# Optimization experiments

Hardware: AMD Instinct MI355X
Metric: run time of the kernel (lower is better)

Reference implementation:

```python
import jax, jax.numpy as jnp
import numpy as np

BN_EPS = 1e-5


def setup_inputs() -> dict:
    key = jax.random.key(0)
    ks = jax.random.split(key, 8)
    N, Cin, Cout, D, H, W = 4, 512, 256, 256, 128, 128
    feat_ffm = jax.random.normal(ks[0], (N, Cin, H, W), dtype=jnp.float32)
    coarse_x = jax.random.normal(ks[1], (N, D, H, W), dtype=jnp.float32)
    # conv1: 1x1, no bias; BN (eval mode: running stats); conv2: 1x1 with bias
    w1 = jax.random.normal(ks[2], (Cout, Cin), dtype=jnp.float32) * (1.0 / np.sqrt(Cin))
    bn_gamma = jnp.ones((Cout,), dtype=jnp.float32)
    bn_beta = jnp.zeros((Cout,), dtype=jnp.float32)
    bn_mean = jax.random.normal(ks[3], (Cout,), dtype=jnp.float32) * 0.1
    bn_var = jax.random.uniform(ks[4], (Cout,), dtype=jnp.float32, minval=0.5, maxval=1.5)
    w2 = jax.random.normal(ks[5], (Cout, Cout), dtype=jnp.float32) * (1.0 / np.sqrt(Cout))
    b2 = jnp.zeros((Cout,), dtype=jnp.float32)
    return {"feat_ffm": feat_ffm, "coarse_x": coarse_x, "w1": w1,
            "bn_gamma": bn_gamma, "bn_beta": bn_beta, "bn_mean": bn_mean,
            "bn_var": bn_var, "w2": w2, "b2": b2}


def reference(feat_ffm, coarse_x, w1, bn_gamma, bn_beta, bn_mean, bn_var, w2, b2):
    N, D, H, W = coarse_x.shape
    # conv1 (1x1) + BN(eval) + ReLU; Dropout2d is identity in eval mode
    x = jnp.einsum('nihw,oi->nohw', feat_ffm, w1)
    scale = bn_gamma * jax.lax.rsqrt(bn_var + BN_EPS)
    x = x * scale[None, :, None, None] + (bn_beta - bn_mean * scale)[None, :, None, None]
    x = jax.nn.relu(x)  # [N, C, H, W]
    C = x.shape[1]
    q = coarse_x.reshape(N, D, H * W)          # proj_query / proj_value
    k = x.reshape(N, C, H * W)                 # proj_key (pre-permute)
    energy = jnp.einsum('nds,ncs->ndc', q, k)  # [N, D, C]
    energy_new = jnp.max(energy, axis=-1, keepdims=True) - energy
    attention = jax.nn.softmax(energy_new, axis=-1)        # [N, D, C]
    out = jnp.einsum('ndc,nds->ncs', attention, q)         # attention^T @ value
    out = out.reshape(N, C, H, W)
    out = jnp.einsum('nchw,oc->nohw', out, w2) + b2[None, :, None, None]
    return out
```

## Files before the change

### kernel.cpp

```cpp
#include <hip/hip_runtime.h>


#define S_DIM 16384
#define C_DIM 256
#define CIN 512

typedef unsigned short u16;
typedef __attribute__((ext_vector_type(8))) short bf16x8;
typedef __attribute__((ext_vector_type(4))) float f32x4;

__device__ __forceinline__ u16 f2bf(float x) {
    unsigned u = __float_as_uint(x);
    u += 0x7fff + ((u >> 16) & 1);
    return (u16)(u >> 16);
}
__device__ __forceinline__ float bf2f(u16 h) {
    return __uint_as_float(((unsigned)h) << 16);
}
__device__ __forceinline__ void gld16(const u16* g, u16* l) {
    __builtin_amdgcn_global_load_lds((const __attribute__((address_space(1))) void*)g,
                                     (__attribute__((address_space(3))) void*)l, 16, 0, 0);
}
__device__ __forceinline__ void gld4(const float* g, float* l) {
    __builtin_amdgcn_global_load_lds((const __attribute__((address_space(1))) void*)g,
                                     (__attribute__((address_space(3))) void*)l, 4, 0, 0);
}

__global__ __launch_bounds__(256) void prep_kernel(
    const float* __restrict__ coarse, const float* __restrict__ w1,
    const float* __restrict__ gamma, const float* __restrict__ beta,
    const float* __restrict__ mean, const float* __restrict__ var,
    u16* __restrict__ qhi, u16* __restrict__ qlo,
    u16* __restrict__ w1hi, u16* __restrict__ w1lo, float* __restrict__ b1) {
    int b = blockIdx.x;
    int t = threadIdx.x;
    if (b < 4096) {
        size_t i = (size_t)b * 256 + t;
        for (size_t c = i; c < 4194304u; c += 1048576u) {
            float4 v = ((const float4*)coarse)[c];
            float vv[4] = {v.x, v.y, v.z, v.w};
            u16 h[4], l[4];
#pragma unroll
            for (int j = 0; j < 4; ++j) {
                h[j] = f2bf(vv[j]);
                l[j] = f2bf(vv[j] - bf2f(h[j]));
            }
            *(uint2*)&qhi[c * 4] = *(uint2*)h;
            *(uint2*)&qlo[c * 4] = *(uint2*)l;
        }
    } else {
        int o = (b - 4096) * 16 + (t >> 4);
        int lane16 = t & 15;
        float sc = gamma[o] * rsqrtf(var[o] + 1e-5f);
        for (int i = lane16; i < CIN; i += 16) {
            float v = w1[o * CIN + i] * sc;
            u16 h = f2bf(v);
            w1hi[o * CIN + i] = h;
            w1lo[o * CIN + i] = f2bf(v - bf2f(h));
        }
        if (lane16 == 0) b1[o] = beta[o] - mean[o] * sc;
    }
}

__global__ __launch_bounds__(256) void conv_kernel(
    const u16* __restrict__ w1hi, const u16* __restrict__ w1lo,
    const float* __restrict__ feat, const float* __restrict__ b1,
    u16* __restrict__ khi, u16* __restrict__ klo) {
    __shared__ u16 AhS[4096], AlS[4096];
    __shared__ float BfS[32 * 133];
    int s0 = blockIdx.x * 128;
    int m0 = blockIdx.y * 128;
    int bz = blockIdx.z;
    int tid = threadIdx.x, wave = tid >> 6, lane = tid & 63;

    int c0 = wave * 128 + lane, c1 = c0 + 64;
    int r0 = c0 >> 2, k0 = (c0 & 3) * 8;
    int r1 = c1 >> 2, k1 = (c1 & 3) * 8;
    const u16* gA0h = w1hi + (size_t)(m0 + r0) * CIN + k0;
    const u16* gA1h = w1hi + (size_t)(m0 + r1) * CIN + k1;
    const u16* gA0l = w1lo + (size_t)(m0 + r0) * CIN + k0;
    const u16* gA1l = w1lo + (size_t)(m0 + r1) * CIN + k1;
    const float* fB = feat + (size_t)bz * ((size_t)CIN * S_DIM) + s0 + lane;

    int quad = lane >> 4, l15 = lane & 15;
    int wm = wave >> 1, wn = wave & 1;
    int aBase = (wm * 64 + l15) * 32 + quad * 8;

    f32x4 zero = {0.f, 0.f, 0.f, 0.f};
    f32x4 acc[4][4];
#pragma unroll
    for (int i = 0; i < 4; ++i)
#pragma unroll
        for (int j = 0; j < 4; ++j) acc[i][j] = zero;

    for (int kb = 0; kb < CIN; kb += 32) {
        __syncthreads();
        gld16(gA0h, AhS + c0 * 8);
        gld16(gA1h, AhS + c1 * 8);
        gld16(gA0l, AlS + c0 * 8);
        gld16(gA1l, AlS + c1 * 8);
        gA0h += 32; gA1h += 32; gA0l += 32; gA1l += 32;
#pragma unroll
        for (int j = 0; j < 16; ++j) {
            int cc = wave * 16 + j;
            int i = cc >> 1, h = cc & 1;
            gld4(fB + (size_t)(kb + i) * S_DIM + h * 64, BfS + i * 133 + h * 64 + lane);
        }
        __syncthreads();

        bf16x8 a_h[4], a_l[4];
#pragma unroll
        for (int t = 0; t < 4; ++t) {
            a_h[t] = *(const bf16x8*)&AhS[aBase + t * 512];
            a_l[t] = *(const bf16x8*)&AlS[aBase + t * 512];
        }
        bf16x8 b_h[4], b_l[4];
#pragma unroll
        for (int nt = 0; nt < 4; ++nt) {
            int n = wn * 64 + nt * 16 + l15;
            union { u16 u[8]; bf16x8 v; } th, tl;
#pragma unroll
            for (int j = 0; j < 8; ++j) {
                float f = BfS[(quad * 8 + j) * 133 + n];
                u16 h = f2bf(f);
                th.u[j] = h;
                tl.u[j] = (u16)(__float_as_uint(f - bf2f(h)) >> 16);
            }
            b_h[nt] = th.v;
            b_l[nt] = tl.v;
        }
#pragma unroll
        for (int mt = 0; mt < 4; ++mt)
#pragma unroll
            for (int nt = 0; nt < 4; ++nt) {
                acc[mt][nt] = __builtin_amdgcn_mfma_f32_16x16x32_bf16(a_h[mt], b_h[nt], acc[mt][nt], 0, 0, 0);
                acc[mt][nt] = __builtin_amdgcn_mfma_f32_16x16x32_bf16(a_h[mt], b_l[nt], acc[mt][nt], 0, 0, 0);
                acc[mt][nt] = __builtin_amdgcn_mfma_f32_16x16x32_bf16(a_l[mt], b_h[nt], acc[mt][nt], 0, 0, 0);
            }
    }

#pragma unroll
    for (int mt = 0; mt < 4; ++mt) {
#pragma unroll
        for (int r = 0; r < 4; ++r) {
            int row = m0 + wm * 64 + mt * 16 + quad * 4 + r;
            float bi = b1[row];
#pragma unroll
            for (int nt = 0; nt < 4; ++nt) {
                int cc = s0 + wn * 64 + nt * 16 + l15;
                float v = fmaxf(acc[mt][nt][r] + bi, 0.f);
                u16 h = f2bf(v);
                size_t o = (size_t)bz * 4194304 + (size_t)row * S_DIM + cc;
                khi[o] = h;
                klo[o] = f2bf(v - bf2f(h));
            }
        }
    }
}

__global__ __launch_bounds__(256) void energy_kernel(
    const u16* __restrict__ qhi, const u16* __restrict__ qlo,
    const u16* __restrict__ khi, const u16* __restrict__ klo,
    float* __restrict__ Ep) {
    __shared__ u16 AhS[4096], BhS[4096], AlS[4096], BlS[4096];
    int kBeg = blockIdx.x * 256;
    int m0 = (blockIdx.y >> 1) * 128;
    int n0 = (blockIdx.y & 1) * 128;
    int bz = blockIdx.z;
    int tid = threadIdx.x, wave = tid >> 6, lane = tid & 63;

    int c0 = wave * 128 + lane, c1 = c0 + 64;
    int r0 = c0 >> 2, k0 = (c0 & 3) * 8;
    int r1 = c1 >> 2, k1 = (c1 & 3) * 8;
    size_t bo = (size_t)bz * 4194304;
    const u16* gA0h = qhi + bo + (size_t)(m0 + r0) * S_DIM + kBeg + k0;
    const u16* gA1h = qhi + bo + (size_t)(m0 + r1) * S_DIM + kBeg + k1;
    const u16* gB0h = khi + bo + (size_t)(n0 + r0) * S_DIM + kBeg + k0;
    const u16* gB1h = khi + bo + (size_t)(n0 + r1) * S_DIM + kBeg + k1;
    const u16* gA0l = qlo + bo + (size_t)(m0 + r0) * S_DIM + kBeg + k0;
    const u16* gA1l = qlo + bo + (size_t)(m0 + r1) * S_DIM + kBeg + k1;
    const u16* gB0l = klo + bo + (size_t)(n0 + r0) * S_DIM + kBeg + k0;
    const u16* gB1l = klo + bo + (size_t)(n0 + r1) * S_DIM + kBeg + k1;

    int quad = lane >> 4, l15 = lane & 15;
    int wm = wave >> 1, wn = wave & 1;
    int aBase = (wm * 64 + l15) * 32 + quad * 8;
    int bBase = (wn * 64 + l15) * 32 + quad * 8;

    f32x4 zero = {0.f, 0.f, 0.f, 0.f};
    f32x4 acc[4][4];
#pragma unroll
    for (int i = 0; i < 4; ++i)
#pragma unroll
        for (int j = 0; j < 4; ++j) acc[i][j] = zero;

    for (int kb = 0; kb < 256; kb += 32) {
        __syncthreads();
        gld16(gA0h, AhS + c0 * 8);
        gld16(gA1h, AhS + c1 * 8);
        gld16(gB0h, BhS + c0 * 8);
        gld16(gB1h, BhS + c1 * 8);
        gld16(gA0l, AlS + c0 * 8);
        gld16(gA1l, AlS + c1 * 8);
        gld16(gB0l, BlS + c0 * 8);
        gld16(gB1l, BlS + c1 * 8);
        gA0h += 32; gA1h += 32; gB0h += 32; gB1h += 32;
        gA0l += 32; gA1l += 32; gB0l += 32; gB1l += 32;
        __syncthreads();

        bf16x8 a_h[4], b_h[4], a_l[4], b_l[4];
#pragma unroll
        for (int t = 0; t < 4; ++t) {
            a_h[t] = *(const bf16x8*)&AhS[aBase + t * 512];
            b_h[t] = *(const bf16x8*)&BhS[bBase + t * 512];
            a_l[t] = *(const bf16x8*)&AlS[aBase + t * 512];
            b_l[t] = *(const bf16x8*)&BlS[bBase + t * 512];
        }
#pragma unroll
        for (int mt = 0; mt < 4; ++mt)
#pragma unroll
            for (int nt = 0; nt < 4; ++nt) {
                acc[mt][nt] = __builtin_amdgcn_mfma_f32_16x16x32_bf16(a_h[mt], b_h[nt], acc[mt][nt], 0, 0, 0);
                acc[mt][nt] = __builtin_amdgcn_mfma_f32_16x16x32_bf16(a_h[mt], b_l[nt], acc[mt][nt], 0, 0, 0);
                acc[mt][nt] = __builtin_amdgcn_mfma_f32_16x16x32_bf16(a_l[mt], b_h[nt], acc[mt][nt], 0, 0, 0);
            }
    }

    float* Ce = Ep + ((size_t)(blockIdx.x * 4 + bz)) * 65536;
#pragma unroll
    for (int mt = 0; mt < 4; ++mt)
#pragma unroll
        for (int r = 0; r < 4; ++r) {
            int row = m0 + wm * 64 + mt * 16 + quad * 4 + r;
#pragma unroll
            for (int nt = 0; nt < 4; ++nt) {
                int cc = n0 + wn * 64 + nt * 16 + l15;
                Ce[(size_t)row * C_DIM + cc] = acc[mt][nt][r];
            }
        }
}

__global__ __launch_bounds__(256) void softmax_kernel(const float* __restrict__ Ep,
                                                      float* __restrict__ att) {
    __shared__ float red[4], red2[4];
    int b = blockIdx.x;
    int t = threadIdx.x;
    const float* p = Ep + (size_t)b * 256 + t;
    float v = 0.f;
#pragma unroll 8
    for (int s = 0; s < 64; ++s) v += p[(size_t)s * 262144];
    float m = v;
#pragma unroll
    for (int o = 32; o > 0; o >>= 1) m = fminf(m, __shfl_xor(m, o, 64));
    int lane = t & 63, wid = t >> 6;
    if (lane == 0) red[wid] = m;
    __syncthreads();
    m = fminf(fminf(red[0], red[1]), fminf(red[2], red[3]));
    float e = expf(m - v);
    float s = e;
#pragma unroll
    for (int o = 32; o > 0; o >>= 1) s += __shfl_xor(s, o, 64);
    if (lane == 0) red2[wid] = s;
    __syncthreads();
    s = red2[0] + red2[1] + red2[2] + red2[3];
    att[(size_t)b * 256 + t] = e / s;
}

__global__ __launch_bounds__(256) void m2h_kernel(const float* __restrict__ w2,
                                                  const float* __restrict__ att,
                                                  u16* __restrict__ M2h) {
    int t = blockIdx.x * 256 + threadIdx.x;
    int d = t & 255, o = (t >> 8) & 255, n = t >> 16;
    const float4* wr = (const float4*)(w2 + (size_t)o * C_DIM);
    const float4* ar = (const float4*)(att + ((size_t)n * C_DIM + d) * C_DIM);
    float s = 0.0f;
#pragma unroll 4
    for (int c4 = 0; c4 < 64; ++c4) {
        float4 w = wr[c4];
        float4 a = ar[c4];
        s += w.x * a.x + w.y * a.y + w.z * a.z + w.w * a.w;
    }
    M2h[((size_t)n * C_DIM + o) * C_DIM + d] = f2bf(s);
}

__global__ __launch_bounds__(256) void final_kernel(
    const u16* __restrict__ M2h, const float* __restrict__ coarse,
    const float* __restrict__ b2, float* __restrict__ out) {
    __shared__ u16 AhS[4096];
    __shared__ float BfS[32 * 133];
    int s0 = blockIdx.x * 128;
    int m0 = blockIdx.y * 128;
    int bz = blockIdx.z;
    int tid = threadIdx.x, wave = tid >> 6, lane = tid & 63;

    int c0 = wave * 128 + lane, c1 = c0 + 64;
    int r0 = c0 >> 2, k0 = (c0 & 3) * 8;
    int r1 = c1 >> 2, k1 = (c1 & 3) * 8;
    const u16* gA0 = M2h + (size_t)bz * 65536 + (size_t)(m0 + r0) * C_DIM + k0;
    const u16* gA1 = M2h + (size_t)bz * 65536 + (size_t)(m0 + r1) * C_DIM + k1;
    const float* fB = coarse + (size_t)bz * 4194304 + s0 + lane;

    int quad = lane >> 4, l15 = lane & 15;
    int wm = wave >> 1, wn = wave & 1;
    int aBase = (wm * 64 + l15) * 32 + quad * 8;

    f32x4 zero = {0.f, 0.f, 0.f, 0.f};
    f32x4 acc[4][4];
#pragma unroll
    for (int i = 0; i < 4; ++i)
#pragma unroll
        for (int j = 0; j < 4; ++j) acc[i][j] = zero;

    for (int kb = 0; kb < C_DIM; kb += 32) {
        __syncthreads();
        gld16(gA0, AhS + c0 * 8);
        gld16(gA1, AhS + c1 * 8);
        gA0 += 32; gA1 += 32;
#pragma unroll
        for (int j = 0; j < 16; ++j) {
            int cc = wave * 16 + j;
            int i = cc >> 1, h = cc & 1;
            gld4(fB + (size_t)(kb + i) * S_DIM + h * 64, BfS + i * 133 + h * 64 + lane);
        }
        __syncthreads();

        bf16x8 a_h[4];
#pragma unroll
        for (int t = 0; t < 4; ++t) a_h[t] = *(const bf16x8*)&AhS[aBase + t * 512];
        bf16x8 b_h[4];
#pragma unroll
        for (int nt = 0; nt < 4; ++nt) {
            int n = wn * 64 + nt * 16 + l15;
            union { u16 u[8]; bf16x8 v; } th;
#pragma unroll
            for (int j = 0; j < 8; ++j) th.u[j] = f2bf(BfS[(quad * 8 + j) * 133 + n]);
            b_h[nt] = th.v;
        }
#pragma unroll
        for (int mt = 0; mt < 4; ++mt)
#pragma unroll
            for (int nt = 0; nt < 4; ++nt)
                acc[mt][nt] = __builtin_amdgcn_mfma_f32_16x16x32_bf16(a_h[mt], b_h[nt], acc[mt][nt], 0, 0, 0);
    }

#pragma unroll
    for (int mt = 0; mt < 4; ++mt)
#pragma unroll
        for (int r = 0; r < 4; ++r) {
            int row = m0 + wm * 64 + mt * 16 + quad * 4 + r;
            float bi = b2[row];
#pragma unroll
            for (int nt = 0; nt < 4; ++nt) {
                int cc = s0 + wn * 64 + nt * 16 + l15;
                out[(size_t)bz * 4194304 + (size_t)row * S_DIM + cc] = acc[mt][nt][r] + bi;
            }
        }
}

extern "C" void kernel_launch(void* const* d_in, const int* in_sizes, int n_in,
                              void* d_out, int out_size, void* d_ws, size_t ws_size,
                              hipStream_t stream) {
    const float* feat   = (const float*)d_in[0];
    const float* coarse = (const float*)d_in[1];
    const float* w1     = (const float*)d_in[2];
    const float* gamma  = (const float*)d_in[3];
    const float* beta   = (const float*)d_in[4];
    const float* mean   = (const float*)d_in[5];
    const float* var    = (const float*)d_in[6];
    const float* w2     = (const float*)d_in[7];
    const float* b2     = (const float*)d_in[8];
    float* out = (float*)d_out;

    char* base = (char*)d_ws;
    u16* qhi   = (u16*)(base);
    u16* qlo   = (u16*)(base + 33554432);
    u16* khi   = (u16*)(base + 67108864);
    u16* klo   = (u16*)(base + 100663296);
    float* Ep  = (float*)(base + 134217728);
    float* att = (float*)(base + 201326592);
    u16* M2h   = (u16*)(base + 202375168);
    u16* w1hi  = (u16*)(base + 202899456);
    u16* w1lo  = (u16*)(base + 203161600);
    float* b1  = (float*)(base + 203423744);

    prep_kernel<<<4112, 256, 0, stream>>>(coarse, w1, gamma, beta, mean, var,
                                          qhi, qlo, w1hi, w1lo, b1);

    conv_kernel<<<dim3(128, 2, 4), 256, 0, stream>>>(w1hi, w1lo, feat, b1, khi, klo);

    energy_kernel<<<dim3(64, 4, 4), 256, 0, stream>>>(qhi, qlo, khi, klo, Ep);

    softmax_kernel<<<1024, 256, 0, stream>>>(Ep, att);

    m2h_kernel<<<1024, 256, 0, stream>>>(w2, att, M2h);

    final_kernel<<<dim3(128, 2, 4), 256, 0, stream>>>(M2h, coarse, b2, out);
}
```

Baseline: 447.5 us.

## Replace LDS staging with direct global loads into MFMA registers

The three GEMM kernels (conv, energy, final) no longer stage operand tiles through shared memory with global_load_lds and barriers. Each lane now loads its MFMA fragments straight from global memory, and the conv kernel's hi/lo split of the fp32 input uses truncation instead of round-to-nearest for the hi part. This removes the LDS traffic and the barriers, but each wave re-reads data from global memory that other waves in the block also load, so more pressure falls on L2. The column-strided fp32 loads issue as many scalar loads per lane.

```diff
diff --git a/kernel.cpp b/kernel.cpp
--- a/kernel.cpp
+++ b/kernel.cpp
@@ -16,14 +16,6 @@
 }
 __device__ __forceinline__ float bf2f(u16 h) {
     return __uint_as_float(((unsigned)h) << 16);
-}
-__device__ __forceinline__ void gld16(const u16* g, u16* l) {
-    __builtin_amdgcn_global_load_lds((const __attribute__((address_space(1))) void*)g,
-                                     (__attribute__((address_space(3))) void*)l, 16, 0, 0);
-}
-__device__ __forceinline__ void gld4(const float* g, float* l) {
-    __builtin_amdgcn_global_load_lds((const __attribute__((address_space(1))) void*)g,
-                                     (__attribute__((address_space(3))) void*)l, 4, 0, 0);
 }
 
 __global__ __launch_bounds__(256) void prep_kernel(
@@ -66,25 +58,17 @@
     const u16* __restrict__ w1hi, const u16* __restrict__ w1lo,
     const float* __restrict__ feat, const float* __restrict__ b1,
     u16* __restrict__ khi, u16* __restrict__ klo) {
-    __shared__ u16 AhS[4096], AlS[4096];
-    __shared__ float BfS[32 * 133];
     int s0 = blockIdx.x * 128;
     int m0 = blockIdx.y * 128;
     int bz = blockIdx.z;
     int tid = threadIdx.x, wave = tid >> 6, lane = tid & 63;
-
-    int c0 = wave * 128 + lane, c1 = c0 + 64;
-    int r0 = c0 >> 2, k0 = (c0 & 3) * 8;
-    int r1 = c1 >> 2, k1 = (c1 & 3) * 8;
-    const u16* gA0h = w1hi + (size_t)(m0 + r0) * CIN + k0;
-    const u16* gA1h = w1hi + (size_t)(m0 + r1) * CIN + k1;
-    const u16* gA0l = w1lo + (size_t)(m0 + r0) * CIN + k0;
-    const u16* gA1l = w1lo + (size_t)(m0 + r1) * CIN + k1;
-    const float* fB = feat + (size_t)bz * ((size_t)CIN * S_DIM) + s0 + lane;
-
     int quad = lane >> 4, l15 = lane & 15;
     int wm = wave >> 1, wn = wave & 1;
-    int aBase = (wm * 64 + l15) * 32 + quad * 8;
+
+    const u16* aH = w1hi + (size_t)(m0 + wm * 64 + l15) * CIN + quad * 8;
+    const u16* aL = w1lo + (size_t)(m0 + wm * 64 + l15) * CIN + quad * 8;
+    const float* fB = feat + (size_t)bz * ((size_t)CIN * S_DIM) +
+                      (size_t)(quad * 8) * S_DIM + s0 + wn * 64 + l15;
 
     f32x4 zero = {0.f, 0.f, 0.f, 0.f};
     f32x4 acc[4][4];
@@ -94,35 +78,22 @@
         for (int j = 0; j < 4; ++j) acc[i][j] = zero;
 
     for (int kb = 0; kb < CIN; kb += 32) {
-        __syncthreads();
-        gld16(gA0h, AhS + c0 * 8);
-        gld16(gA1h, AhS + c1 * 8);
-        gld16(gA0l, AlS + c0 * 8);
-        gld16(gA1l, AlS + c1 * 8);
-        gA0h += 32; gA1h += 32; gA0l += 32; gA1l += 32;
-#pragma unroll
-        for (int j = 0; j < 16; ++j) {
-            int cc = wave * 16 + j;
-            int i = cc >> 1, h = cc & 1;
-            gld4(fB + (size_t)(kb + i) * S_DIM + h * 64, BfS + i * 133 + h * 64 + lane);
-        }
-        __syncthreads();
-
         bf16x8 a_h[4], a_l[4];
 #pragma unroll
-        for (int t = 0; t < 4; ++t) {
-            a_h[t] = *(const bf16x8*)&AhS[aBase + t * 512];
-            a_l[t] = *(const bf16x8*)&AlS[aBase + t * 512];
-        }
+        for (int mt = 0; mt < 4; ++mt) {
+            a_h[mt] = *(const bf16x8*)&aH[(size_t)(mt * 16) * CIN + kb];
+            a_l[mt] = *(const bf16x8*)&aL[(size_t)(mt * 16) * CIN + kb];
+        }
+        const float* fk = fB + (size_t)kb * S_DIM;
         bf16x8 b_h[4], b_l[4];
 #pragma unroll
         for (int nt = 0; nt < 4; ++nt) {
-            int n = wn * 64 + nt * 16 + l15;
             union { u16 u[8]; bf16x8 v; } th, tl;
 #pragma unroll
             for (int j = 0; j < 8; ++j) {
-                float f = BfS[(quad * 8 + j) * 133 + n];
-                u16 h = f2bf(f);
+                float f = fk[(size_t)j * S_DIM + nt * 16];
+                unsigned u = __float_as_uint(f);
+                u16 h = (u16)(u >> 16);
                 th.u[j] = h;
                 tl.u[j] = (u16)(__float_as_uint(f - bf2f(h)) >> 16);
             }
@@ -140,7 +111,7 @@
     }
 
 #pragma unroll
-    for (int mt = 0; mt < 4; ++mt) {
+    for (int mt = 0; mt < 4; ++mt)
 #pragma unroll
         for (int r = 0; r < 4; ++r) {
             int row = m0 + wm * 64 + mt * 16 + quad * 4 + r;
@@ -155,37 +126,25 @@
                 klo[o] = f2bf(v - bf2f(h));
             }
         }
-    }
 }
 
 __global__ __launch_bounds__(256) void energy_kernel(
     const u16* __restrict__ qhi, const u16* __restrict__ qlo,
     const u16* __restrict__ khi, const u16* __restrict__ klo,
     float* __restrict__ Ep) {
-    __shared__ u16 AhS[4096], BhS[4096], AlS[4096], BlS[4096];
     int kBeg = blockIdx.x * 256;
     int m0 = (blockIdx.y >> 1) * 128;
     int n0 = (blockIdx.y & 1) * 128;
     int bz = blockIdx.z;
     int tid = threadIdx.x, wave = tid >> 6, lane = tid & 63;
-
-    int c0 = wave * 128 + lane, c1 = c0 + 64;
-    int r0 = c0 >> 2, k0 = (c0 & 3) * 8;
-    int r1 = c1 >> 2, k1 = (c1 & 3) * 8;
-    size_t bo = (size_t)bz * 4194304;
-    const u16* gA0h = qhi + bo + (size_t)(m0 + r0) * S_DIM + kBeg + k0;
-    const u16* gA1h = qhi + bo + (size_t)(m0 + r1) * S_DIM + kBeg + k1;
-    const u16* gB0h = khi + bo + (size_t)(n0 + r0) * S_DIM + kBeg + k0;
-    const u16* gB1h = khi + bo + (size_t)(n0 + r1) * S_DIM + kBeg + k1;
-    const u16* gA0l = qlo + bo + (size_t)(m0 + r0) * S_DIM + kBeg + k0;
-    const u16* gA1l = qlo + bo + (size_t)(m0 + r1) * S_DIM + kBeg + k1;
-    const u16* gB0l = klo + bo + (size_t)(n0 + r0) * S_DIM + kBeg + k0;
-    const u16* gB1l = klo + bo + (size_t)(n0 + r1) * S_DIM + kBeg + k1;
-
     int quad = lane >> 4, l15 = lane & 15;
     int wm = wave >> 1, wn = wave & 1;
-    int aBase = (wm * 64 + l15) * 32 + quad * 8;
-    int bBase = (wn * 64 + l15) * 32 + quad * 8;
+
+    size_t bo = (size_t)bz * 4194304;
+    const u16* aH = qhi + bo + (size_t)(m0 + wm * 64 + l15) * S_DIM + kBeg + quad * 8;
+    const u16* aL = qlo + bo + (size_t)(m0 + wm * 64 + l15) * S_DIM + kBeg + quad * 8;
+    const u16* bH = khi + bo + (size_t)(n0 + wn * 64 + l15) * S_DIM + kBeg + quad * 8;
+    const u16* bL = klo + bo + (size_t)(n0 + wn * 64 + l15) * S_DIM + kBeg + quad * 8;
 
     f32x4 zero = {0.f, 0.f, 0.f, 0.f};
     f32x4 acc[4][4];
@@ -195,26 +154,13 @@
         for (int j = 0; j < 4; ++j) acc[i][j] = zero;
 
     for (int kb = 0; kb < 256; kb += 32) {
-        __syncthreads();
-        gld16(gA0h, AhS + c0 * 8);
-        gld16(gA1h, AhS + c1 * 8);
-        gld16(gB0h, BhS + c0 * 8);
-        gld16(gB1h, BhS + c1 * 8);
-        gld16(gA0l, AlS + c0 * 8);
-        gld16(gA1l, AlS + c1 * 8);
-        gld16(gB0l, BlS + c0 * 8);
-        gld16(gB1l, BlS + c1 * 8);
-        gA0h += 32; gA1h += 32; gB0h += 32; gB1h += 32;
-        gA0l += 32; gA1l += 32; gB0l += 32; gB1l += 32;
-        __syncthreads();
-
-        bf16x8 a_h[4], b_h[4], a_l[4], b_l[4];
+        bf16x8 a_h[4], a_l[4], b_h[4], b_l[4];
 #pragma unroll
         for (int t = 0; t < 4; ++t) {
-            a_h[t] = *(const bf16x8*)&AhS[aBase + t * 512];
-            b_h[t] = *(const bf16x8*)&BhS[bBase + t * 512];
-            a_l[t] = *(const bf16x8*)&AlS[aBase + t * 512];
-            b_l[t] = *(const bf16x8*)&BlS[bBase + t * 512];
+            a_h[t] = *(const bf16x8*)&aH[(size_t)(t * 16) * S_DIM + kb];
+            a_l[t] = *(const bf16x8*)&aL[(size_t)(t * 16) * S_DIM + kb];
+            b_h[t] = *(const bf16x8*)&bH[(size_t)(t * 16) * S_DIM + kb];
+            b_l[t] = *(const bf16x8*)&bL[(size_t)(t * 16) * S_DIM + kb];
         }
 #pragma unroll
         for (int mt = 0; mt < 4; ++mt)
@@ -286,23 +232,16 @@
 __global__ __launch_bounds__(256) void final_kernel(
     const u16* __restrict__ M2h, const float* __restrict__ coarse,
     const float* __restrict__ b2, float* __restrict__ out) {
-    __shared__ u16 AhS[4096];
-    __shared__ float BfS[32 * 133];
     int s0 = blockIdx.x * 128;
     int m0 = blockIdx.y * 128;
     int bz = blockIdx.z;
     int tid = threadIdx.x, wave = tid >> 6, lane = tid & 63;
-
-    int c0 = wave * 128 + lane, c1 = c0 + 64;
-    int r0 = c0 >> 2, k0 = (c0 & 3) * 8;
-    int r1 = c1 >> 2, k1 = (c1 & 3) * 8;
-    const u16* gA0 = M2h + (size_t)bz * 65536 + (size_t)(m0 + r0) * C_DIM + k0;
-    const u16* gA1 = M2h + (size_t)bz * 65536 + (size_t)(m0 + r1) * C_DIM + k1;
-    const float* fB = coarse + (size_t)bz * 4194304 + s0 + lane;
-
     int quad = lane >> 4, l15 = lane & 15;
     int wm = wave >> 1, wn = wave & 1;
-    int aBase = (wm * 64 + l15) * 32 + quad * 8;
+
+    const u16* aH = M2h + (size_t)bz * 65536 + (size_t)(m0 + wm * 64 + l15) * C_DIM + quad * 8;
+    const float* fB = coarse + (size_t)bz * 4194304 +
+                      (size_t)(quad * 8) * S_DIM + s0 + wn * 64 + l15;
 
     f32x4 zero = {0.f, 0.f, 0.f, 0.f};
     f32x4 acc[4][4];
@@ -312,28 +251,17 @@
         for (int j = 0; j < 4; ++j) acc[i][j] = zero;
 
     for (int kb = 0; kb < C_DIM; kb += 32) {
-        __syncthreads();
-        gld16(gA0, AhS + c0 * 8);
-        gld16(gA1, AhS + c1 * 8);
-        gA0 += 32; gA1 += 32;
-#pragma unroll
-        for (int j = 0; j < 16; ++j) {
-            int cc = wave * 16 + j;
-            int i = cc >> 1, h = cc & 1;
-            gld4(fB + (size_t)(kb + i) * S_DIM + h * 64, BfS + i * 133 + h * 64 + lane);
-        }
-        __syncthreads();
-
         bf16x8 a_h[4];
 #pragma unroll
-        for (int t = 0; t < 4; ++t) a_h[t] = *(const bf16x8*)&AhS[aBase + t * 512];
+        for (int mt = 0; mt < 4; ++mt)
+            a_h[mt] = *(const bf16x8*)&aH[(size_t)(mt * 16) * C_DIM + kb];
+        const float* fk = fB + (size_t)kb * S_DIM;
         bf16x8 b_h[4];
 #pragma unroll
         for (int nt = 0; nt < 4; ++nt) {
-            int n = wn * 64 + nt * 16 + l15;
             union { u16 u[8]; bf16x8 v; } th;
 #pragma unroll
-            for (int j = 0; j < 8; ++j) th.u[j] = f2bf(BfS[(quad * 8 + j) * 133 + n]);
+            for (int j = 0; j < 8; ++j) th.u[j] = f2bf(fk[(size_t)j * S_DIM + nt * 16]);
             b_h[nt] = th.v;
         }
 #pragma unroll
```

Measured after the change: 532.7 us. +19.0%, slower.
